# Performance work log

Hardware: AMD Instinct MI355X
Metric: run time of the kernel (lower is better)

## Reference

```python
import jax, jax.numpy as jnp
import numpy as np

POOL = 2  # maxout pool size


def setup_inputs() -> dict:
    key = jax.random.key(0)
    ks = jax.random.split(key, 20)
    V, WV, ENC, DEC, ATT = 32000, 512, 512, 512, 512
    T, B, S, L = 32, 64, 256, 1
    IN = WV + ENC  # input_feed: emb concat context
    sc = 0.02
    emb_table = jax.random.normal(ks[0], (V, WV), jnp.float32) * sc
    emb_table = emb_table.at[0].set(0.0)  # padding_idx = PAD = 0
    inp = {
        'input_ids': jax.random.randint(ks[1], (T, B), 0, V),
        'hidden': jax.random.normal(ks[2], (L, B, DEC), jnp.float32),
        'context': jax.random.normal(ks[3], (S, B, ENC), jnp.float32),
        'src_pad_mask': jnp.zeros((B, S), jnp.float32),
        'init_att': jax.random.normal(ks[4], (B, ENC), jnp.float32),
        'emb_table': emb_table,
        'W_ih': jax.random.normal(ks[5], (3 * DEC, IN), jnp.float32) * sc,
        'W_hh': jax.random.normal(ks[6], (3 * DEC, DEC), jnp.float32) * sc,
        'b_ih': jnp.zeros((3 * DEC,), jnp.float32),
        'b_hh': jnp.zeros((3 * DEC,), jnp.float32),
        'W_pre': jax.random.normal(ks[7], (ATT, ENC), jnp.float32) * sc,
        'b_pre': jnp.zeros((ATT,), jnp.float32),
        'W_q': jax.random.normal(ks[8], (ATT, DEC), jnp.float32) * sc,
        'v_att': jax.random.normal(ks[9], (ATT,), jnp.float32) * sc,
        'W_copy': jax.random.normal(ks[10], (1, ENC + DEC), jnp.float32) * sc,
        'b_copy': jnp.zeros((1,), jnp.float32),
        'W_read': jax.random.normal(ks[11], (DEC, ENC + DEC + WV), jnp.float32) * sc,
        'b_read': jnp.zeros((DEC,), jnp.float32),
    }
    return inp


def reference(input_ids, hidden, context, src_pad_mask, init_att, emb_table,
              W_ih, W_hh, b_ih, b_hh, W_pre, b_pre, W_q, v_att,
              W_copy, b_copy, W_read, b_read):
    T, B = input_ids.shape
    dec = hidden.shape[-1]
    ctx_t = jnp.transpose(context, (1, 0, 2))            # [B, S, enc]
    # ConcatAttention precompute (done once, reused each step)
    precompute = jnp.einsum('bse,ae->bsa', ctx_t, W_pre) + b_pre  # [B, S, att]
    emb = emb_table[input_ids]                           # [T, B, wv]

    def gru_cell(x, h):
        gx = x @ W_ih.T + b_ih
        gh = h @ W_hh.T + b_hh
        xr, xz, xn = jnp.split(gx, 3, axis=-1)
        hr, hz, hn = jnp.split(gh, 3, axis=-1)
        r = jax.nn.sigmoid(xr + hr)
        z = jax.nn.sigmoid(xz + hz)
        n = jnp.tanh(xn + r * hn)
        return (1.0 - z) * n + z * h

    def step(carry, emb_t):
        h, cur_ctx = carry                               # h: [1,B,dec]
        x = jnp.concatenate([emb_t, cur_ctx], axis=1)    # input_feed
        h_new = gru_cell(x, h[0])
        out = h_new                                      # single layer output
        # concat attention
        target = out @ W_q.T                             # [B, att]
        tmp = jnp.tanh(precompute + target[:, None, :])  # [B, S, att]
        energy = jnp.einsum('bsa,a->bs', tmp, v_att)
        energy = energy * (1.0 - src_pad_mask) + src_pad_mask * (-1e6)
        score = jax.nn.softmax(energy, axis=-1)          # [B, S]
        new_ctx = jnp.einsum('bs,bse->be', score, ctx_t)
        # copy gate
        copy_p = jax.nn.sigmoid(
            jnp.concatenate([out, new_ctx], axis=1) @ W_copy.T + b_copy)
        # readout + maxout (dropout is identity at eval)
        readout = jnp.concatenate([emb_t, out, new_ctx], axis=1) @ W_read.T + b_read
        mo = readout.reshape(B, dec // POOL, POOL).max(axis=-1)
        return (h_new[None], new_ctx), (mo, score, copy_p)

    (hid, cur_ctx), (g_out, c_out, copy_out) = jax.lax.scan(
        step, (hidden, init_att), emb)
    return g_out, c_out, copy_out, hid, c_out[-1], cur_ctx
```

## Files before the change

kernel.cpp:

```cpp
#include <hip/hip_runtime.h>
#include <hip/hip_bf16.h>


typedef unsigned int uint;
typedef unsigned short ushort;
typedef __attribute__((ext_vector_type(8))) short s8v;
typedef __attribute__((ext_vector_type(4))) float f4v;

#define DD 512

__device__ __forceinline__ float sigmf(float x) { return 1.0f / (1.0f + __expf(-x)); }
__device__ __forceinline__ float tanh_fast(float x) {
    float e = __expf(2.0f * x);
    return 1.0f - 2.0f / (e + 1.0f);
}
__device__ __forceinline__ ushort f2bf(float f) {
    uint b = __float_as_uint(f);
    return (ushort)((b + 0x7FFFu + ((b >> 16) & 1u)) >> 16);
}
__device__ __forceinline__ uint pk2(float a, float b) {
    return (uint)f2bf(a) | ((uint)f2bf(b) << 16);
}
__device__ __forceinline__ float bfl(uint u) { return __uint_as_float(u << 16); }
__device__ __forceinline__ float bfh(uint u) { return __uint_as_float(u & 0xFFFF0000u); }
__device__ __forceinline__ f4v MFMA(s8v a, s8v b, f4v c) {
    return __builtin_amdgcn_mfma_f32_16x16x32_bf16(a, b, c, 0, 0, 0);
}

__device__ __forceinline__ void flag_bar(uint* arr, uint* rel, int member,
                                         int nmem, uint tag) {
    __syncthreads();
    const int tid = threadIdx.x;
    if (tid == 0) {
        asm volatile("s_waitcnt vmcnt(0) lgkmcnt(0)" ::: "memory");
        __hip_atomic_store(arr + member, tag, __ATOMIC_RELAXED,
                           __HIP_MEMORY_SCOPE_AGENT);
    }
    if (member == 0) {
        if (tid > 0 && tid < nmem) {
            while (__hip_atomic_load(arr + tid, __ATOMIC_RELAXED,
                                     __HIP_MEMORY_SCOPE_AGENT) < tag) {}
        }
        if (tid == 0)
            __hip_atomic_store(rel, tag, __ATOMIC_RELAXED,
                               __HIP_MEMORY_SCOPE_AGENT);
    } else {
        if (tid == 0) {
            while (__hip_atomic_load(rel, __ATOMIC_RELAXED,
                                     __HIP_MEMORY_SCOPE_AGENT) < tag) {}
        }
    }
    __syncthreads();
}

template <int MODE, int MT>
__global__ __launch_bounds__(256) void mgemm(
    const float* __restrict__ A0, const float* __restrict__ A1,
    const float* __restrict__ A2, const int* __restrict__ ids,
    const float* __restrict__ Bm, const float* __restrict__ bias,
    void* __restrict__ Cout, int ldb, int K)
{
    __shared__ __align__(16) ushort Ab[MT * 16 * 32];
    __shared__ __align__(16) ushort Bb[64 * 32];
    __shared__ int rid[MT * 16];
    const int tid = threadIdx.x;
    const int m0 = blockIdx.x * (MT * 16), n0 = blockIdx.y * 64;
    if (MODE != 0 && tid < MT * 16) rid[tid] = ids[m0 + tid];
    const int lane = tid & 63;
    const int w = tid >> 6;
    const int sc = tid & 3;
    f4v acc[MT];
#pragma unroll
    for (int mt = 0; mt < MT; ++mt) acc[mt] = (f4v){0.f, 0.f, 0.f, 0.f};

    for (int k0 = 0; k0 < K; k0 += 32) {
        __syncthreads();
#pragma unroll
        for (int p = 0; p < MT / 4; ++p) {
            int row = p * 64 + (tid >> 2);
            const float* ap;
            int m = m0 + row;
            if (MODE == 0) {
                ap = A0 + (size_t)(m & 255) * 32768 + (size_t)(m >> 8) * 512 + k0 + sc * 8;
            } else if (MODE == 1) {
                ap = A0 + (size_t)rid[row] * 512 + k0 + sc * 8;
            } else {
                if (k0 < 512)       ap = A0 + (size_t)rid[row] * 512 + k0 + sc * 8;
                else if (k0 < 1024) ap = A1 + (size_t)m * 512 + (k0 - 512) + sc * 8;
                else                ap = A2 + (size_t)m * 512 + (k0 - 1024) + sc * 8;
            }
            float4 v0 = *(const float4*)ap;
            float4 v1 = *(const float4*)(ap + 4);
            uint4 pa;
            pa.x = pk2(v0.x, v0.y); pa.y = pk2(v0.z, v0.w);
            pa.z = pk2(v1.x, v1.y); pa.w = pk2(v1.z, v1.w);
            *(uint4*)&Ab[row * 32 + ((sc ^ (row & 3)) << 3)] = pa;
        }
        {
            int row = tid >> 2;
            const float* bp = Bm + (size_t)(n0 + row) * ldb + k0 + sc * 8;
            float4 w0 = *(const float4*)bp;
            float4 w1 = *(const float4*)(bp + 4);
            uint4 pb;
            pb.x = pk2(w0.x, w0.y); pb.y = pk2(w0.z, w0.w);
            pb.z = pk2(w1.x, w1.y); pb.w = pk2(w1.z, w1.w);
            *(uint4*)&Bb[row * 32 + ((sc ^ (row & 3)) << 3)] = pb;
        }
        __syncthreads();
        int rr = lane & 15, kc = lane >> 4;
        s8v bf = *(const s8v*)&Bb[(w * 16 + rr) * 32 + ((kc ^ (rr & 3)) << 3)];
#pragma unroll
        for (int mt = 0; mt < MT; ++mt) {
            s8v af = *(const s8v*)&Ab[(mt * 16 + rr) * 32 + ((kc ^ (rr & 3)) << 3)];
            acc[mt] = MFMA(af, bf, acc[mt]);
        }
    }
    float bv = bias[n0 + w * 16 + (lane & 15)];
#pragma unroll
    for (int mt = 0; mt < MT; ++mt) {
#pragma unroll
        for (int r2 = 0; r2 < 4; ++r2) {
            int m = m0 + mt * 16 + (lane >> 4) * 4 + r2;
            int n = n0 + w * 16 + (lane & 15);
            float v = acc[mt][r2] + bv;
            if (MODE == 0) {
                ((ushort*)Cout)[(size_t)m * 512 + n] = f2bf(v);
            } else if (MODE == 1) {
                ((float*)Cout)[(size_t)m * 1536 + n] = v;
            } else {
                float vm = fmaxf(v, __shfl_xor(v, 1));
                if (!(lane & 1)) ((float*)Cout)[(size_t)m * 256 + (n >> 1)] = vm;
            }
        }
    }
}

__global__ __launch_bounds__(512) void wprep2(
    const float* __restrict__ W_ih, const float* __restrict__ W_hh,
    const float* __restrict__ W_q,
    uint* __restrict__ Wpk, uint* __restrict__ WqT)
{
    int id = blockIdx.x * 512 + threadIdx.x;
    if (id < 786432) {
        int l4 = id & 255;
        int chunk = id >> 8;
        int g = chunk % 3;
        int t2 = chunk / 3;
        int ks = t2 & 15;
        int mat = (t2 >> 4) & 1;
        int u = t2 >> 5;
        int lane = l4 >> 2, e2 = l4 & 3;
        int n = g * 512 + u * 16 + (lane & 15);
        int k = ks * 32 + ((lane >> 4) << 3) + e2 * 2;
        float w0, w1;
        if (mat == 0) {
            w0 = W_ih[(size_t)n * 1024 + 512 + k];
            w1 = W_ih[(size_t)n * 1024 + 512 + k + 1];
        } else {
            w0 = W_hh[(size_t)n * 512 + k];
            w1 = W_hh[(size_t)n * 512 + k + 1];
        }
        Wpk[id] = pk2(w0, w1);
    } else if (id < 917504) {
        int rid2 = id - 786432;
        int kp = rid2 >> 9, a = rid2 & 511;
        WqT[rid2] = pk2(W_q[(size_t)a * 512 + 2 * kp], W_q[(size_t)a * 512 + 2 * kp + 1]);
    }
}

__global__ __launch_bounds__(512, 1) void k_steps(
    const float* __restrict__ gxe, const float* __restrict__ hidden,
    const float* __restrict__ init_att, const float* __restrict__ context,
    const float* __restrict__ mask, const float* __restrict__ v_att,
    const float* __restrict__ b_hh, const ushort* __restrict__ preb,
    const uint* __restrict__ Wpk, const uint* __restrict__ WqT,
    float* __restrict__ h_hist, float* __restrict__ ctx_hist,
    float* __restrict__ pe_buf, uint* __restrict__ cnt,
    float* __restrict__ cout)
{
    __shared__ __align__(16) ushort preT[256 * 128];
    __shared__ __align__(16) ushort ctxT[256 * 128];
    __shared__ __align__(16) float scr[6144];
    __shared__ float smask[256];
    __shared__ float svatt[128];

    const int tid = threadIdx.x;
    const int blk = blockIdx.x;
    const int q = blk >> 6;
    const int b = blk & 63;
    const int r = b & 7;
    const int u = ((b >> 3) << 2) | q;
    const int lane = tid & 63;
    const int wid = __builtin_amdgcn_readfirstlane(tid >> 6);

    uint* garr = cnt + r * 64;
    uint* grel = cnt + 512 + r * 16;
    uint* carr = cnt + 1024 + b * 8;
    uint* crel = cnt + 2048 + b * 16;

#pragma unroll
    for (int cc = 0; cc < 8; ++cc) {
        int cid = tid * 8 + cc;
        int s = cid >> 4, ch = cid & 15;
        int sw = (s ^ (s >> 3)) & 7;
        uint4 pv = *(const uint4*)(preb + ((size_t)(b * 256 + s)) * 512 + q * 128 + ch * 8);
        *(uint4*)&preT[s * 128 + ((ch ^ sw) << 3)] = pv;
        const float* cp = context + ((size_t)s * 64 + b) * 512 + q * 128 + ch * 8;
        float4 c0 = *(const float4*)cp;
        float4 c1 = *(const float4*)(cp + 4);
        uint4 cv;
        cv.x = pk2(c0.x, c0.y); cv.y = pk2(c0.z, c0.w);
        cv.z = pk2(c1.x, c1.y); cv.w = pk2(c1.z, c1.w);
        *(uint4*)&ctxT[s * 128 + ch * 8] = cv;
    }
    if (tid < 256) smask[tid] = mask[b * 256 + tid];
    else if (tid < 384) svatt[tid - 256] = v_att[q * 128 + (tid - 256)];

    const int mat_w = wid >> 2, kw = wid & 3;
    s8v wr0[4], wr1[4], wr2[4];
#pragma unroll
    for (int s = 0; s < 4; ++s) {
        int ks = kw * 4 + s;
        const uint* wb = Wpk + ((((u * 2 + mat_w) * 16 + ks) * 3) << 8) + (lane << 2);
        wr0[s] = *(const s8v*)(wb);
        wr1[s] = *(const s8v*)(wb + 256);
        wr2[s] = *(const s8v*)(wb + 512);
    }
    const int a_p2 = tid & 127, dq_p2 = tid >> 7;
    uint wqreg[64];
#pragma unroll
    for (int i = 0; i < 64; ++i)
        wqreg[i] = WqT[(size_t)(dq_p2 * 64 + i) * 512 + q * 128 + a_p2];

    const int bloc = tid >> 4, jj = tid & 15;
    int bb_c = 0, d_c = 0, eidx = 0;
    float bh0 = 0.f, bh1 = 0.f, bh2 = 0.f;
    if (tid < 128) {
        bb_c = r + bloc * 8;
        d_c = u * 16 + jj;
        eidx = ((jj + ((bloc >> 2) << 4)) << 2) + (bloc & 3);
        bh0 = b_hh[d_c]; bh1 = b_hh[512 + d_c]; bh2 = b_hh[1024 + d_c];
    }

    for (int t = 0; t < 32; ++t) {
        const float* ctxp = t ? (ctx_hist + (size_t)(t - 1) * 32768) : init_att;
        const float* hp = t ? (h_hist + (size_t)(t - 1) * 32768) : hidden;

        float gx0 = 0.f, gx1 = 0.f, gx2 = 0.f, hpv = 0.f;
        if (tid < 128) {
            const float* gp = gxe + ((size_t)t * 64 + bb_c) * 1536 + d_c;
            gx0 = gp[0]; gx1 = gp[512]; gx2 = gp[1024];
            hpv = hp[(size_t)bb_c * 512 + d_c];
        }

        __syncthreads();
        {
            int c2 = tid & 31, row = (tid >> 5) & 7, mat = tid >> 8;
            const float* src = mat ? hp : ctxp;
            int bb = r + row * 8;
            const float* sp = src + (size_t)bb * 512 + c2 * 16;
            float4 v0 = *(const float4*)sp, v1 = *(const float4*)(sp + 4);
            float4 v2 = *(const float4*)(sp + 8), v3 = *(const float4*)(sp + 12);
            uint4 p0, p1;
            p0.x = pk2(v0.x, v0.y); p0.y = pk2(v0.z, v0.w);
            p0.z = pk2(v1.x, v1.y); p0.w = pk2(v1.z, v1.w);
            p1.x = pk2(v2.x, v2.y); p1.y = pk2(v2.z, v2.w);
            p1.z = pk2(v3.x, v3.y); p1.w = pk2(v3.z, v3.w);
            char* xb = (char*)scr + mat * 8192 + row * 1024;
            int c0 = c2 * 2;
            *(uint4*)(xb + ((c0 ^ row) << 4)) = p0;
            *(uint4*)(xb + (((c0 + 1) ^ row) << 4)) = p1;
        }
        __syncthreads();
        f4v ac0 = (f4v){0.f, 0.f, 0.f, 0.f};
        f4v ac1 = ac0, ac2 = ac0;
        {
            const char* xbase = (const char*)scr + mat_w * 8192 + (lane & 15) * 1024;
            int rsw = (lane & 15) & 7;
#pragma unroll
            for (int s = 0; s < 4; ++s) {
                int ch = kw * 16 + s * 4 + (lane >> 4);
                s8v af = *(const s8v*)(xbase + ((ch ^ rsw) << 4));
                ac0 = MFMA(af, wr0[s], ac0);
                ac1 = MFMA(af, wr1[s], ac1);
                ac2 = MFMA(af, wr2[s], ac2);
            }
        }
        __syncthreads();
        {
            f4v* rb = (f4v*)scr;
            rb[((mat_w * 3 + 0) * 4 + kw) * 64 + lane] = ac0;
            rb[((mat_w * 3 + 1) * 4 + kw) * 64 + lane] = ac1;
            rb[((mat_w * 3 + 2) * 4 + kw) * 64 + lane] = ac2;
        }
        __syncthreads();
        if (tid < 128) {
            float AX[3], AH[3];
#pragma unroll
            for (int g = 0; g < 3; ++g) {
                float sx = 0.f, sh = 0.f;
#pragma unroll
                for (int kw2 = 0; kw2 < 4; ++kw2) {
                    sx += scr[((0 + g) * 4 + kw2) * 256 + eidx];
                    sh += scr[((3 + g) * 4 + kw2) * 256 + eidx];
                }
                AX[g] = sx;
                AH[g] = sh;
            }
            AX[0] += gx0; AX[1] += gx1; AX[2] += gx2;
            AH[0] += bh0; AH[1] += bh1; AH[2] += bh2;
            float rr = sigmf(AX[0] + AH[0]);
            float zz = sigmf(AX[1] + AH[1]);
            float nn = tanh_fast(AX[2] + rr * AH[2]);
            h_hist[(size_t)t * 32768 + (size_t)bb_c * 512 + d_c] =
                (1.0f - zz) * nn + zz * hpv;
        }
        flag_bar(garr, grel, u, 32, (uint)(t * 4 + 1));

        scr[tid] = h_hist[(size_t)t * 32768 + (size_t)b * 512 + tid];
        __syncthreads();
        {
            float acc = 0.f;
#pragma unroll
            for (int i = 0; i < 64; ++i) {
                uint w = wqreg[i];
                acc = fmaf(bfl(w), scr[(dq_p2 * 64 + i) * 2 + 0],
                           fmaf(bfh(w), scr[(dq_p2 * 64 + i) * 2 + 1], acc));
            }
            scr[512 + tid] = acc;
        }
        __syncthreads();
        if (tid < 128)
            scr[1024 + tid] = scr[512 + tid] + scr[640 + tid] +
                              scr[768 + tid] + scr[896 + tid];
        __syncthreads();

        {
            int s = tid & 255, hf = tid >> 8;
            int sw = (s ^ (s >> 3)) & 7;
            float acc0 = 0.f, acc1 = 0.f;
#pragma unroll
            for (int c8 = 0; c8 < 8; ++c8) {
                int ch = hf * 8 + c8;
                uint4 pv = *(const uint4*)&preT[s * 128 + ((ch ^ sw) << 3)];
                int ab = ch * 8;
                acc0 += svatt[ab + 0] * tanh_fast(bfl(pv.x) + scr[1024 + ab + 0]);
                acc1 += svatt[ab + 1] * tanh_fast(bfh(pv.x) + scr[1024 + ab + 1]);
                acc0 += svatt[ab + 2] * tanh_fast(bfl(pv.y) + scr[1024 + ab + 2]);
                acc1 += svatt[ab + 3] * tanh_fast(bfh(pv.y) + scr[1024 + ab + 3]);
                acc0 += svatt[ab + 4] * tanh_fast(bfl(pv.z) + scr[1024 + ab + 4]);
                acc1 += svatt[ab + 5] * tanh_fast(bfh(pv.z) + scr[1024 + ab + 5]);
                acc0 += svatt[ab + 6] * tanh_fast(bfl(pv.w) + scr[1024 + ab + 6]);
                acc1 += svatt[ab + 7] * tanh_fast(bfh(pv.w) + scr[1024 + ab + 7]);
            }
            scr[1280 + tid] = acc0 + acc1;
        }
        __syncthreads();
        if (tid < 256)
            pe_buf[((size_t)t * 64 + b) * 1024 + q * 256 + tid] =
                scr[1280 + tid] + scr[1536 + tid];
        flag_bar(carr, crel, q, 4, (uint)(t * 4 + 2));

        {
            int s2 = tid & 255;
            const float* peb = pe_buf + ((size_t)t * 64 + b) * 1024;
            float e = peb[s2] + peb[256 + s2] + peb[512 + s2] + peb[768 + s2];
            float mk = smask[s2];
            e = e * (1.0f - mk) + mk * (-1e6f);
            float mx = e;
#pragma unroll
            for (int off = 1; off < 64; off <<= 1) mx = fmaxf(mx, __shfl_xor(mx, off));
            if (lane == 0) scr[3072 + wid] = mx;
            __syncthreads();
            mx = scr[3072];
#pragma unroll
            for (int w2 = 1; w2 < 8; ++w2) mx = fmaxf(mx, scr[3072 + w2]);
            float ex = __expf(e - mx);
            float sm = ex;
#pragma unroll
            for (int off = 1; off < 64; off <<= 1) sm += __shfl_xor(sm, off);
            if (lane == 0) scr[3080 + wid] = sm;
            __syncthreads();
            sm = scr[3080] + scr[3081] + scr[3082] + scr[3083];
            scr[1792 + s2] = ex / sm;
        }
        __syncthreads();
        if (tid < 64)
            cout[((size_t)t * 64 + b) * 256 + q * 64 + tid] = scr[1792 + q * 64 + tid];
        {
            int e2 = tid & 63, sq = tid >> 6;
            float acc0 = 0.f, acc1 = 0.f;
#pragma unroll 8
            for (int i = 0; i < 32; ++i) {
                int ss = sq * 32 + i;
                uint cv = *(const uint*)&ctxT[ss * 128 + e2 * 2];
                float sc = scr[1792 + ss];
                acc0 = fmaf(sc, bfl(cv), acc0);
                acc1 = fmaf(sc, bfh(cv), acc1);
            }
            scr[2048 + sq * 128 + e2 * 2 + 0] = acc0;
            scr[2048 + sq * 128 + e2 * 2 + 1] = acc1;
        }
        __syncthreads();
        if (tid < 128) {
            float val = 0.f;
#pragma unroll
            for (int s8 = 0; s8 < 8; ++s8) val += scr[2048 + s8 * 128 + tid];
            ctx_hist[(size_t)t * 32768 + (size_t)b * 512 + q * 128 + tid] = val;
        }
        flag_bar(garr, grel, u, 32, (uint)(t * 4 + 3));
    }
}

__global__ __launch_bounds__(256) void k_copy(
    const float* __restrict__ h_hist, const float* __restrict__ ctx_hist,
    const float* __restrict__ W_copy, const float* __restrict__ b_copy,
    float* __restrict__ out)
{
    const int tid = threadIdx.x;
    const int lane = tid & 63;
    const int tb = blockIdx.x * 4 + (tid >> 6);
    const float* hp = h_hist + (size_t)tb * DD;
    const float* cp = ctx_hist + (size_t)tb * DD;
    float acc = 0.f;
#pragma unroll
    for (int jj = 0; jj < 8; ++jj) {
        int k = lane + 64 * jj;
        acc = fmaf(hp[k], W_copy[k], acc);
        acc = fmaf(cp[k], W_copy[512 + k], acc);
    }
#pragma unroll
    for (int off = 1; off < 64; off <<= 1) acc += __shfl_xor(acc, off);
    if (lane == 0) out[tb] = sigmf(acc + b_copy[0]);
}

__global__ void k_final(const float* __restrict__ h_hist,
                        const float* __restrict__ ctx_hist,
                        float* __restrict__ dout)
{
    int idx = blockIdx.x * 256 + threadIdx.x;
    if (idx < 32768) {
        dout[1050624 + idx] = h_hist[31 * 32768 + idx];
    } else if (idx < 49152) {
        int i2 = idx - 32768;
        dout[1083392 + i2] = dout[524288 + 507904 + i2];
    } else {
        int i2 = idx - 49152;
        dout[1099776 + i2] = ctx_hist[31 * 32768 + i2];
    }
}

extern "C" void kernel_launch(void* const* d_in, const int* in_sizes, int n_in,
                              void* d_out, int out_size, void* d_ws, size_t ws_size,
                              hipStream_t stream)
{
    (void)in_sizes; (void)n_in; (void)out_size; (void)ws_size;
    const int*   ids      = (const int*)d_in[0];
    const float* hidden   = (const float*)d_in[1];
    const float* context  = (const float*)d_in[2];
    const float* mask     = (const float*)d_in[3];
    const float* init_att = (const float*)d_in[4];
    const float* emb_t    = (const float*)d_in[5];
    const float* W_ih     = (const float*)d_in[6];
    const float* W_hh     = (const float*)d_in[7];
    const float* b_ih     = (const float*)d_in[8];
    const float* b_hh     = (const float*)d_in[9];
    const float* W_pre    = (const float*)d_in[10];
    const float* b_pre    = (const float*)d_in[11];
    const float* W_q      = (const float*)d_in[12];
    const float* v_att    = (const float*)d_in[13];
    const float* W_copy   = (const float*)d_in[14];
    const float* b_copy   = (const float*)d_in[15];
    const float* W_read   = (const float*)d_in[16];
    const float* b_read   = (const float*)d_in[17];
    float* out = (float*)d_out;
    float* ws = (float*)d_ws;

    ushort* preb    = (ushort*)ws;
    float* gxe      = ws + 4194304;
    float* h_hist   = ws + 7340032;
    float* ctx_hist = ws + 8388608;
    float* pe_buf   = ws + 9437184;
    uint* Wpk       = (uint*)(ws + 11534336);
    uint* WqT       = (uint*)(ws + 12320768);
    uint* cnt       = (uint*)(ws + 12451840);
    float* cout     = out + 524288;

    hipMemsetAsync(cnt, 0, 16384, stream);
    mgemm<0, 8><<<dim3(128, 8), 256, 0, stream>>>(context, nullptr, nullptr, nullptr,
                                                  W_pre, b_pre, (void*)preb, 512, 512);
    mgemm<1, 4><<<dim3(32, 24), 256, 0, stream>>>(emb_t, nullptr, nullptr, ids,
                                                  W_ih, b_ih, (void*)gxe, 1024, 512);
    wprep2<<<1792, 512, 0, stream>>>(W_ih, W_hh, W_q, Wpk, WqT);
    {
        void* args[] = {
            (void*)&gxe, (void*)&hidden, (void*)&init_att, (void*)&context,
            (void*)&mask, (void*)&v_att, (void*)&b_hh, (void*)&preb,
            (void*)&Wpk, (void*)&WqT,
            (void*)&h_hist, (void*)&ctx_hist, (void*)&pe_buf, (void*)&cnt,
            (void*)&cout
        };
        hipLaunchCooperativeKernel((void*)k_steps, dim3(256), dim3(512), args, 0,
                                   stream);
    }
    mgemm<2, 4><<<dim3(32, 8), 256, 0, stream>>>(emb_t, h_hist, ctx_hist, ids,
                                                 W_read, b_read, (void*)out, 1536, 1536);
    k_copy<<<512, 256, 0, stream>>>(h_hist, ctx_hist, W_copy, b_copy, out + 1048576);
    k_final<<<320, 256, 0, stream>>>(h_hist, ctx_hist, out);
}
```

Measured before the change: 666.1 us.

## Merge prep/post kernels and overlap next-step loads with grid barrier

Fuses the precompute GEMMs, weight packing and counter reset into one launch, and the readout GEMM, copy gate and final copies into another, to cut launch overhead. Inside the recurrent cooperative kernel, the next step's gate inputs and hidden state are loaded and packed to shared memory between the arrival signal and the barrier wait, hiding some load latency behind the sync. The attention score store is folded into the softmax stage and the tanh accumulation uses a single accumulator, which lengthens a dependency chain.

```diff
diff --git a/kernel.cpp b/kernel.cpp
--- a/kernel.cpp
+++ b/kernel.cpp
@@ -54,17 +54,15 @@
 }
 
 template <int MODE, int MT>
-__global__ __launch_bounds__(256) void mgemm(
+__device__ __forceinline__ void mgemm_body(
     const float* __restrict__ A0, const float* __restrict__ A1,
     const float* __restrict__ A2, const int* __restrict__ ids,
     const float* __restrict__ Bm, const float* __restrict__ bias,
-    void* __restrict__ Cout, int ldb, int K)
+    void* __restrict__ Cout, int ldb, int K, int bx, int by,
+    ushort* Ab, ushort* Bb, int* rid)
 {
-    __shared__ __align__(16) ushort Ab[MT * 16 * 32];
-    __shared__ __align__(16) ushort Bb[64 * 32];
-    __shared__ int rid[MT * 16];
     const int tid = threadIdx.x;
-    const int m0 = blockIdx.x * (MT * 16), n0 = blockIdx.y * 64;
+    const int m0 = bx * (MT * 16), n0 = by * 64;
     if (MODE != 0 && tid < MT * 16) rid[tid] = ids[m0 + tid];
     const int lane = tid & 63;
     const int w = tid >> 6;
@@ -135,36 +133,58 @@
     }
 }
 
-__global__ __launch_bounds__(512) void wprep2(
+__global__ __launch_bounds__(256) void k_prep(
+    const float* __restrict__ context, const float* __restrict__ emb_t,
+    const int* __restrict__ ids,
     const float* __restrict__ W_ih, const float* __restrict__ W_hh,
-    const float* __restrict__ W_q,
-    uint* __restrict__ Wpk, uint* __restrict__ WqT)
+    const float* __restrict__ W_q, const float* __restrict__ W_pre,
+    const float* __restrict__ b_pre, const float* __restrict__ b_ih,
+    ushort* __restrict__ preb, float* __restrict__ gxe,
+    uint* __restrict__ Wpk, uint* __restrict__ WqT, uint* __restrict__ cnt)
 {
-    int id = blockIdx.x * 512 + threadIdx.x;
-    if (id < 786432) {
-        int l4 = id & 255;
-        int chunk = id >> 8;
-        int g = chunk % 3;
-        int t2 = chunk / 3;
-        int ks = t2 & 15;
-        int mat = (t2 >> 4) & 1;
-        int u = t2 >> 5;
-        int lane = l4 >> 2, e2 = l4 & 3;
-        int n = g * 512 + u * 16 + (lane & 15);
-        int k = ks * 32 + ((lane >> 4) << 3) + e2 * 2;
-        float w0, w1;
-        if (mat == 0) {
-            w0 = W_ih[(size_t)n * 1024 + 512 + k];
-            w1 = W_ih[(size_t)n * 1024 + 512 + k + 1];
+    __shared__ __align__(16) ushort Ab[8 * 16 * 32];
+    __shared__ __align__(16) ushort Bb[64 * 32];
+    __shared__ int rid[128];
+    const int bid = blockIdx.x;
+    if (bid < 1024) {
+        mgemm_body<0, 8>(context, nullptr, nullptr, nullptr, W_pre, b_pre,
+                         (void*)preb, 512, 512, bid & 127, bid >> 7, Ab, Bb, rid);
+    } else if (bid < 1792) {
+        int b2 = bid - 1024;
+        mgemm_body<1, 4>(emb_t, nullptr, nullptr, ids, W_ih, b_ih,
+                         (void*)gxe, 1024, 512, b2 & 31, b2 >> 5, Ab, Bb, rid);
+    } else if (bid < 5376) {
+        int id = (bid - 1792) * 256 + threadIdx.x;
+        if (id < 786432) {
+            int l4 = id & 255;
+            int chunk = id >> 8;
+            int g = chunk % 3;
+            int t2 = chunk / 3;
+            int ks = t2 & 15;
+            int mat = (t2 >> 4) & 1;
+            int u = t2 >> 5;
+            int lane = l4 >> 2, e2 = l4 & 3;
+            int n = g * 512 + u * 16 + (lane & 15);
+            int k = ks * 32 + ((lane >> 4) << 3) + e2 * 2;
+            float w0, w1;
+            if (mat == 0) {
+                w0 = W_ih[(size_t)n * 1024 + 512 + k];
+                w1 = W_ih[(size_t)n * 1024 + 512 + k + 1];
+            } else {
+                w0 = W_hh[(size_t)n * 512 + k];
+                w1 = W_hh[(size_t)n * 512 + k + 1];
+            }
+            Wpk[id] = pk2(w0, w1);
         } else {
-            w0 = W_hh[(size_t)n * 512 + k];
-            w1 = W_hh[(size_t)n * 512 + k + 1];
-        }
-        Wpk[id] = pk2(w0, w1);
-    } else if (id < 917504) {
-        int rid2 = id - 786432;
-        int kp = rid2 >> 9, a = rid2 & 511;
-        WqT[rid2] = pk2(W_q[(size_t)a * 512 + 2 * kp], W_q[(size_t)a * 512 + 2 * kp + 1]);
+            int rid2 = id - 786432;
+            int kp = rid2 >> 9, a = rid2 & 511;
+            WqT[rid2] = pk2(W_q[(size_t)a * 512 + 2 * kp],
+                            W_q[(size_t)a * 512 + 2 * kp + 1]);
+        }
+    } else {
+        int t4 = threadIdx.x * 16;
+#pragma unroll
+        for (int i = 0; i < 16; ++i) cnt[t4 + i] = 0;
     }
 }
 
@@ -242,36 +262,31 @@
         bh0 = b_hh[d_c]; bh1 = b_hh[512 + d_c]; bh2 = b_hh[1024 + d_c];
     }
 
+    float gx0 = 0.f, gx1 = 0.f, gx2 = 0.f, hpv = 0.f;
+    if (tid < 128) {
+        const float* gp = gxe + (size_t)bb_c * 1536 + d_c;
+        gx0 = gp[0]; gx1 = gp[512]; gx2 = gp[1024];
+        hpv = hidden[(size_t)bb_c * 512 + d_c];
+    }
+    {
+        int c = tid & 63, row = tid >> 6;
+        int bb = r + row * 8;
+        const float* sp0 = init_att + (size_t)bb * 512 + c * 8;
+        float4 a0 = *(const float4*)sp0, a1 = *(const float4*)(sp0 + 4);
+        uint4 p0;
+        p0.x = pk2(a0.x, a0.y); p0.y = pk2(a0.z, a0.w);
+        p0.z = pk2(a1.x, a1.y); p0.w = pk2(a1.z, a1.w);
+        *(uint4*)((char*)scr + row * 1024 + ((c ^ row) << 4)) = p0;
+        const float* sp1 = hidden + (size_t)bb * 512 + c * 8;
+        float4 b0 = *(const float4*)sp1, b1 = *(const float4*)(sp1 + 4);
+        uint4 p1;
+        p1.x = pk2(b0.x, b0.y); p1.y = pk2(b0.z, b0.w);
+        p1.z = pk2(b1.x, b1.y); p1.w = pk2(b1.z, b1.w);
+        *(uint4*)((char*)scr + 8192 + row * 1024 + ((c ^ row) << 4)) = p1;
+    }
+    __syncthreads();
+
     for (int t = 0; t < 32; ++t) {
-        const float* ctxp = t ? (ctx_hist + (size_t)(t - 1) * 32768) : init_att;
-        const float* hp = t ? (h_hist + (size_t)(t - 1) * 32768) : hidden;
-
-        float gx0 = 0.f, gx1 = 0.f, gx2 = 0.f, hpv = 0.f;
-        if (tid < 128) {
-            const float* gp = gxe + ((size_t)t * 64 + bb_c) * 1536 + d_c;
-            gx0 = gp[0]; gx1 = gp[512]; gx2 = gp[1024];
-            hpv = hp[(size_t)bb_c * 512 + d_c];
-        }
-
-        __syncthreads();
-        {
-            int c2 = tid & 31, row = (tid >> 5) & 7, mat = tid >> 8;
-            const float* src = mat ? hp : ctxp;
-            int bb = r + row * 8;
-            const float* sp = src + (size_t)bb * 512 + c2 * 16;
-            float4 v0 = *(const float4*)sp, v1 = *(const float4*)(sp + 4);
-            float4 v2 = *(const float4*)(sp + 8), v3 = *(const float4*)(sp + 12);
-            uint4 p0, p1;
-            p0.x = pk2(v0.x, v0.y); p0.y = pk2(v0.z, v0.w);
-            p0.z = pk2(v1.x, v1.y); p0.w = pk2(v1.z, v1.w);
-            p1.x = pk2(v2.x, v2.y); p1.y = pk2(v2.z, v2.w);
-            p1.z = pk2(v3.x, v3.y); p1.w = pk2(v3.z, v3.w);
-            char* xb = (char*)scr + mat * 8192 + row * 1024;
-            int c0 = c2 * 2;
-            *(uint4*)(xb + ((c0 ^ row) << 4)) = p0;
-            *(uint4*)(xb + (((c0 + 1) ^ row) << 4)) = p1;
-        }
-        __syncthreads();
         f4v ac0 = (f4v){0.f, 0.f, 0.f, 0.f};
         f4v ac1 = ac0, ac2 = ac0;
         {
@@ -338,22 +353,22 @@
         {
             int s = tid & 255, hf = tid >> 8;
             int sw = (s ^ (s >> 3)) & 7;
-            float acc0 = 0.f, acc1 = 0.f;
+            float acc = 0.f;
 #pragma unroll
             for (int c8 = 0; c8 < 8; ++c8) {
                 int ch = hf * 8 + c8;
                 uint4 pv = *(const uint4*)&preT[s * 128 + ((ch ^ sw) << 3)];
                 int ab = ch * 8;
-                acc0 += svatt[ab + 0] * tanh_fast(bfl(pv.x) + scr[1024 + ab + 0]);
-                acc1 += svatt[ab + 1] * tanh_fast(bfh(pv.x) + scr[1024 + ab + 1]);
-                acc0 += svatt[ab + 2] * tanh_fast(bfl(pv.y) + scr[1024 + ab + 2]);
-                acc1 += svatt[ab + 3] * tanh_fast(bfh(pv.y) + scr[1024 + ab + 3]);
-                acc0 += svatt[ab + 4] * tanh_fast(bfl(pv.z) + scr[1024 + ab + 4]);
-                acc1 += svatt[ab + 5] * tanh_fast(bfh(pv.z) + scr[1024 + ab + 5]);
-                acc0 += svatt[ab + 6] * tanh_fast(bfl(pv.w) + scr[1024 + ab + 6]);
-                acc1 += svatt[ab + 7] * tanh_fast(bfh(pv.w) + scr[1024 + ab + 7]);
-            }
-            scr[1280 + tid] = acc0 + acc1;
+                acc += svatt[ab + 0] * tanh_fast(bfl(pv.x) + scr[1024 + ab + 0]);
+                acc += svatt[ab + 1] * tanh_fast(bfh(pv.x) + scr[1024 + ab + 1]);
+                acc += svatt[ab + 2] * tanh_fast(bfl(pv.y) + scr[1024 + ab + 2]);
+                acc += svatt[ab + 3] * tanh_fast(bfh(pv.y) + scr[1024 + ab + 3]);
+                acc += svatt[ab + 4] * tanh_fast(bfl(pv.z) + scr[1024 + ab + 4]);
+                acc += svatt[ab + 5] * tanh_fast(bfh(pv.z) + scr[1024 + ab + 5]);
+                acc += svatt[ab + 6] * tanh_fast(bfl(pv.w) + scr[1024 + ab + 6]);
+                acc += svatt[ab + 7] * tanh_fast(bfh(pv.w) + scr[1024 + ab + 7]);
+            }
+            scr[1280 + tid] = acc;
         }
         __syncthreads();
         if (tid < 256)
@@ -382,11 +397,11 @@
             if (lane == 0) scr[3080 + wid] = sm;
             __syncthreads();
             sm = scr[3080] + scr[3081] + scr[3082] + scr[3083];
-            scr[1792 + s2] = ex / sm;
-        }
-        __syncthreads();
-        if (tid < 64)
-            cout[((size_t)t * 64 + b) * 256 + q * 64 + tid] = scr[1792 + q * 64 + tid];
+            float sc = ex / sm;
+            scr[1792 + s2] = sc;
+            if (q == 0 && tid < 256) cout[((size_t)t * 64 + b) * 256 + tid] = sc;
+        }
+        __syncthreads();
         {
             int e2 = tid & 63, sq = tid >> 6;
             float acc0 = 0.f, acc1 = 0.f;
@@ -408,45 +423,98 @@
             for (int s8 = 0; s8 < 8; ++s8) val += scr[2048 + s8 * 128 + tid];
             ctx_hist[(size_t)t * 32768 + (size_t)b * 512 + q * 128 + tid] = val;
         }
-        flag_bar(garr, grel, u, 32, (uint)(t * 4 + 3));
-    }
-}
-
-__global__ __launch_bounds__(256) void k_copy(
+
+        __syncthreads();
+        if (tid == 0) {
+            asm volatile("s_waitcnt vmcnt(0) lgkmcnt(0)" ::: "memory");
+            __hip_atomic_store(garr + u, (uint)(t * 4 + 3), __ATOMIC_RELAXED,
+                               __HIP_MEMORY_SCOPE_AGENT);
+        }
+        if (t < 31) {
+            if (tid < 128) {
+                const float* gp = gxe + ((size_t)(t + 1) * 64 + bb_c) * 1536 + d_c;
+                gx0 = gp[0]; gx1 = gp[512]; gx2 = gp[1024];
+                hpv = h_hist[(size_t)t * 32768 + (size_t)bb_c * 512 + d_c];
+            }
+            int c = tid & 63, row = tid >> 6;
+            int bb = r + row * 8;
+            const float* sp = h_hist + (size_t)t * 32768 + (size_t)bb * 512 + c * 8;
+            float4 v0 = *(const float4*)sp, v1 = *(const float4*)(sp + 4);
+            uint4 p1;
+            p1.x = pk2(v0.x, v0.y); p1.y = pk2(v0.z, v0.w);
+            p1.z = pk2(v1.x, v1.y); p1.w = pk2(v1.z, v1.w);
+            *(uint4*)((char*)scr + 8192 + row * 1024 + ((c ^ row) << 4)) = p1;
+        }
+        if (u == 0) {
+            if (tid > 0 && tid < 32) {
+                while (__hip_atomic_load(garr + tid, __ATOMIC_RELAXED,
+                                         __HIP_MEMORY_SCOPE_AGENT) < (uint)(t * 4 + 3)) {}
+            }
+            if (tid == 0)
+                __hip_atomic_store(grel, (uint)(t * 4 + 3), __ATOMIC_RELAXED,
+                                   __HIP_MEMORY_SCOPE_AGENT);
+        } else {
+            if (tid == 0) {
+                while (__hip_atomic_load(grel, __ATOMIC_RELAXED,
+                                         __HIP_MEMORY_SCOPE_AGENT) < (uint)(t * 4 + 3)) {}
+            }
+        }
+        __syncthreads();
+        if (t < 31) {
+            int c = tid & 63, row = tid >> 6;
+            int bb = r + row * 8;
+            const float* sp = ctx_hist + (size_t)t * 32768 + (size_t)bb * 512 + c * 8;
+            float4 v0 = *(const float4*)sp, v1 = *(const float4*)(sp + 4);
+            uint4 p0;
+            p0.x = pk2(v0.x, v0.y); p0.y = pk2(v0.z, v0.w);
+            p0.z = pk2(v1.x, v1.y); p0.w = pk2(v1.z, v1.w);
+            *(uint4*)((char*)scr + row * 1024 + ((c ^ row) << 4)) = p0;
+        }
+        __syncthreads();
+    }
+}
+
+__global__ __launch_bounds__(256) void k_post(
+    const float* __restrict__ emb_t, const int* __restrict__ ids,
     const float* __restrict__ h_hist, const float* __restrict__ ctx_hist,
+    const float* __restrict__ W_read, const float* __restrict__ b_read,
     const float* __restrict__ W_copy, const float* __restrict__ b_copy,
     float* __restrict__ out)
 {
+    __shared__ __align__(16) ushort Ab[4 * 16 * 32];
+    __shared__ __align__(16) ushort Bb[64 * 32];
+    __shared__ int rid[64];
+    const int bid = blockIdx.x;
     const int tid = threadIdx.x;
-    const int lane = tid & 63;
-    const int tb = blockIdx.x * 4 + (tid >> 6);
-    const float* hp = h_hist + (size_t)tb * DD;
-    const float* cp = ctx_hist + (size_t)tb * DD;
-    float acc = 0.f;
-#pragma unroll
-    for (int jj = 0; jj < 8; ++jj) {
-        int k = lane + 64 * jj;
-        acc = fmaf(hp[k], W_copy[k], acc);
-        acc = fmaf(cp[k], W_copy[512 + k], acc);
-    }
-#pragma unroll
-    for (int off = 1; off < 64; off <<= 1) acc += __shfl_xor(acc, off);
-    if (lane == 0) out[tb] = sigmf(acc + b_copy[0]);
-}
-
-__global__ void k_final(const float* __restrict__ h_hist,
-                        const float* __restrict__ ctx_hist,
-                        float* __restrict__ dout)
-{
-    int idx = blockIdx.x * 256 + threadIdx.x;
-    if (idx < 32768) {
-        dout[1050624 + idx] = h_hist[31 * 32768 + idx];
-    } else if (idx < 49152) {
-        int i2 = idx - 32768;
-        dout[1083392 + i2] = dout[524288 + 507904 + i2];
+    if (bid < 256) {
+        mgemm_body<2, 4>(emb_t, h_hist, ctx_hist, ids, W_read, b_read,
+                         (void*)out, 1536, 1536, bid & 31, bid >> 5, Ab, Bb, rid);
+    } else if (bid < 768) {
+        const int lane = tid & 63;
+        const int tb = (bid - 256) * 4 + (tid >> 6);
+        const float* hp = h_hist + (size_t)tb * DD;
+        const float* cp = ctx_hist + (size_t)tb * DD;
+        float acc = 0.f;
+#pragma unroll
+        for (int jj = 0; jj < 8; ++jj) {
+            int k = lane + 64 * jj;
+            acc = fmaf(hp[k], W_copy[k], acc);
+            acc = fmaf(cp[k], W_copy[512 + k], acc);
+        }
+#pragma unroll
+        for (int off = 1; off < 64; off <<= 1) acc += __shfl_xor(acc, off);
+        if (lane == 0) out[1048576 + tb] = sigmf(acc + b_copy[0]);
     } else {
-        int i2 = idx - 49152;
-        dout[1099776 + i2] = ctx_hist[31 * 32768 + i2];
+        int idx = (bid - 768) * 256 + tid;
+        if (idx < 32768) {
+            out[1050624 + idx] = h_hist[31 * 32768 + idx];
+        } else if (idx < 49152) {
+            int i2 = idx - 32768;
+            out[1083392 + i2] = out[524288 + 507904 + i2];
+        } else {
+            int i2 = idx - 49152;
+            out[1099776 + i2] = ctx_hist[31 * 32768 + i2];
+        }
     }
 }
 
@@ -486,12 +554,8 @@
     uint* cnt       = (uint*)(ws + 12451840);
     float* cout     = out + 524288;
 
-    hipMemsetAsync(cnt, 0, 16384, stream);
-    mgemm<0, 8><<<dim3(128, 8), 256, 0, stream>>>(context, nullptr, nullptr, nullptr,
-                                                  W_pre, b_pre, (void*)preb, 512, 512);
-    mgemm<1, 4><<<dim3(32, 24), 256, 0, stream>>>(emb_t, nullptr, nullptr, ids,
-                                                  W_ih, b_ih, (void*)gxe, 1024, 512);
-    wprep2<<<1792, 512, 0, stream>>>(W_ih, W_hh, W_q, Wpk, WqT);
+    k_prep<<<5377, 256, 0, stream>>>(context, emb_t, ids, W_ih, W_hh, W_q, W_pre,
+                                     b_pre, b_ih, preb, gxe, Wpk, WqT, cnt);
     {
         void* args[] = {
             (void*)&gxe, (void*)&hidden, (void*)&init_att, (void*)&context,
@@ -503,8 +567,6 @@
         hipLaunchCooperativeKernel((void*)k_steps, dim3(256), dim3(512), args, 0,
                                    stream);
     }
-    mgemm<2, 4><<<dim3(32, 8), 256, 0, stream>>>(emb_t, h_hist, ctx_hist, ids,
-                                                 W_read, b_read, (void*)out, 1536, 1536);
-    k_copy<<<512, 256, 0, stream>>>(h_hist, ctx_hist, W_copy, b_copy, out + 1048576);
-    k_final<<<320, 256, 0, stream>>>(h_hist, ctx_hist, out);
-}
+    k_post<<<1088, 256, 0, stream>>>(emb_t, ids, h_hist, ctx_hist, W_read, b_read,
+                                     W_copy, b_copy, out);
+}
```

Result: faster. 556.3 us, median of 3 (-16.5%).
